# Kernel optimization log

Hardware: AMD Instinct MI355X
Metric: run time of the kernel (lower is better)

## Reference

```python
import jax, jax.numpy as jnp
import numpy as np

N_HEAD, N_MIX, D_MODEL, D_K, D_V = 8, 2, 512, 64, 64
BN_EPS = 1e-5


def avg_pool_3x3_s2(x):
    # AvgPool2d(kernel=3, stride=2, pad=1, count_include_pad=False) on NCHW
    win = (1, 1, 3, 3)
    stride = (1, 1, 2, 2)
    pad = [(0, 0), (0, 0), (1, 1), (1, 1)]
    s = jax.lax.reduce_window(x, 0.0, jax.lax.add, win, stride, pad)
    ones = jnp.ones((1, 1, x.shape[2], x.shape[3]), x.dtype)
    cnt = jax.lax.reduce_window(ones, 0.0, jax.lax.add, win, stride, pad)
    return s / cnt


def conv1x1(x, w, b=None):
    # w: [out_c, in_c]; x: [B, in_c, H, W]
    y = jnp.einsum('oc,bchw->bohw', w, x)
    if b is not None:
        y = y + b[None, :, None, None]
    return y


def setup_inputs() -> dict:
    key = jax.random.key(0)
    ks = jax.random.split(key, 8)
    B, H, W = 2, 56, 56
    std_kq = np.sqrt(2.0 / (D_MODEL + D_K)).astype(np.float32)
    std_v = np.sqrt(2.0 / (D_MODEL + D_V)).astype(np.float32)
    std_mix = np.power(N_MIX, -0.5).astype(np.float32)
    return {
        'x': jax.random.normal(ks[0], (B, D_MODEL, H, W), jnp.float32),
        'w_qs': jax.random.normal(ks[1], (N_HEAD * D_K, D_MODEL), jnp.float32) * std_kq,
        'b_qs': jnp.zeros((N_HEAD * D_K,), jnp.float32),
        'w_vs': jax.random.normal(ks[2], (N_HEAD * D_V, D_MODEL), jnp.float32) * std_v,
        'b_vs': jnp.zeros((N_HEAD * D_V,), jnp.float32),
        'mix_w': jax.random.uniform(ks[3], (N_MIX, D_K), jnp.float32, -std_mix, std_mix),
        'w_out': jax.random.normal(ks[4], (D_MODEL, N_HEAD * D_V), jnp.float32) * 0.02,
        'bn_gamma': jnp.ones((D_MODEL,), jnp.float32),
        'bn_beta': jnp.zeros((D_MODEL,), jnp.float32),
    }


def reference(x, w_qs, b_qs, w_vs, b_vs, mix_w, w_out, bn_gamma, bn_beta):
    B, C, H, W = x.shape
    N = H * W
    m = N_MIX
    d = D_K // m  # per-mixture dim
    temperature = D_K ** 0.5

    px = avg_pool_3x3_s2(x)  # [B, C, H/2, W/2]
    N2 = px.shape[2] * px.shape[3]

    # conv_ks aliases conv_qs in the original (shared weights)
    qt = conv1x1(x, w_qs, b_qs).reshape(B * N_HEAD, D_K, N)
    kt = conv1x1(px, w_qs, b_qs).reshape(B * N_HEAD, D_K, N2)
    vt = conv1x1(px, w_vs, b_vs).reshape(B * N_HEAD, D_V, N2)

    # mixture weights pi: softmax over mixtures of weight @ mean_q
    bar_qt = qt.mean(axis=2)  # [B', D_K]
    pi = jax.nn.softmax(jnp.einsum('md,bd->bm', mix_w, bar_qt), axis=1)  # [B', m]

    q = qt.reshape(B * N_HEAD * m, d, N).transpose(0, 2, 1)  # [B'm, N, d]
    k2 = kt.reshape(B * N_HEAD * m, d, N2)  # [B'm, d, N2]

    attn = jnp.einsum('bnd,bdk->bnk', q, k2) / temperature  # [B'm, N, N2]
    attn = jax.nn.softmax(attn, axis=2)
    # dropout is identity in eval mode
    attn = (attn * pi.reshape(-1, 1, 1)).reshape(B * N_HEAD, m, N, N2).sum(1)

    out = jnp.einsum('bnk,bvk->bnv', attn, vt)  # [B', N, D_V]
    out = out.transpose(0, 2, 1).reshape(B, N_HEAD * D_V, H, W)
    out = conv1x1(out, w_out)  # no bias
    # BatchNorm2d in eval mode: running_mean=0, running_var=1
    inv = 1.0 / jnp.sqrt(jnp.float32(1.0 + BN_EPS))
    out = out * inv * bn_gamma[None, :, None, None] + bn_beta[None, :, None, None]
    return out + x
```

## Files before the change

kernel.cpp:

```cpp
#include <hip/hip_runtime.h>
#include <math.h>

typedef unsigned short u16;
typedef short bf16x8 __attribute__((ext_vector_type(8)));
typedef short bf16x4 __attribute__((ext_vector_type(4)));
typedef float f32x4 __attribute__((ext_vector_type(4)));

#define MFMA(a, b, c) __builtin_amdgcn_mfma_f32_16x16x32_bf16(a, b, c, 0, 0, 0)

#define SCALE_K 0.18033688011112043f

__device__ __forceinline__ float bf2f(u16 v) {
    union { float f; unsigned u; } x;
    x.u = ((unsigned)v) << 16;
    return x.f;
}
__device__ __forceinline__ u16 f2bf(float f) {
    union { float f; unsigned u; } x;
    x.f = f;
    unsigned r = x.u + 0x7FFF + ((x.u >> 16) & 1);
    return (u16)(r >> 16);
}
__device__ __forceinline__ bf16x4 pk4(float a, float b, float c, float d) {
    union { unsigned u[2]; bf16x4 v; } x;
    asm("v_cvt_pk_bf16_f32 %0, %1, %2" : "=v"(x.u[0]) : "v"(a), "v"(b));
    asm("v_cvt_pk_bf16_f32 %0, %1, %2" : "=v"(x.u[1]) : "v"(c), "v"(d));
    return x.v;
}

__global__ __launch_bounds__(256) void cvt_kernel(const float* __restrict__ s0,
                                                  const float* __restrict__ s1,
                                                  const float* __restrict__ s2,
                                                  u16* __restrict__ d0, u16* __restrict__ d1,
                                                  u16* __restrict__ d2) {
    int i = blockIdx.x * 256 + threadIdx.x;
    const float* s = (blockIdx.y == 0) ? s0 : ((blockIdx.y == 1) ? s1 : s2);
    u16* d = (blockIdx.y == 0) ? d0 : ((blockIdx.y == 1) ? d1 : d2);
    d[i] = f2bf(s[i]);
}

__global__ __launch_bounds__(256) void transpose_kernel(const float* __restrict__ x,
                                                        u16* __restrict__ xT) {
    __shared__ u16 tile[64][65];
    int b = blockIdx.z;
    int n0 = blockIdx.x * 64, c0 = blockIdx.y * 64;
    int j = threadIdx.x & 63, q = threadIdx.x >> 6;
    const float* xb = x + b * 512 * 3136;
#pragma unroll
    for (int it = 0; it < 16; ++it) {
        int r = q * 16 + it;
        tile[r][j] = f2bf(xb[(c0 + r) * 3136 + n0 + j]);
    }
    __syncthreads();
    u16* xTb = xT + b * 3136 * 512;
#pragma unroll
    for (int it = 0; it < 16; ++it) {
        int r = q * 16 + it;
        xTb[(n0 + r) * 512 + c0 + j] = tile[j][r];
    }
}

__global__ __launch_bounds__(256) void pool_kernel(const u16* __restrict__ xT,
                                                   u16* __restrict__ pxT) {
    int n2 = blockIdx.x;
    int b = blockIdx.y;
    int t = threadIdx.x;
    int i = n2 / 28, jj = n2 % 28;
    float s0 = 0.f, s1 = 0.f;
    int cnt = 0;
    const u16* xb = xT + b * 3136 * 512;
#pragma unroll
    for (int dr = 0; dr < 3; dr++) {
        int r = 2 * i - 1 + dr;
        if (r < 0 || r >= 56) continue;
#pragma unroll
        for (int dc = 0; dc < 3; dc++) {
            int cc = 2 * jj - 1 + dc;
            if (cc < 0 || cc >= 56) continue;
            const u16* row = xb + (r * 56 + cc) * 512;
            s0 += bf2f(row[t]);
            s1 += bf2f(row[t + 256]);
            cnt++;
        }
    }
    float invc = 1.0f / (float)cnt;
    u16* op = pxT + (b * 784 + n2) * 512;
    op[t] = f2bf(s0 * invc);
    op[t + 256] = f2bf(s1 * invc);
}

__device__ __forceinline__ void gemm_core(const u16* __restrict__ A, int lda, int M,
                                          const u16* __restrict__ BT, int ldb, int Ncol,
                                          int K, int row0, int col0, f32x4 acc[4][4]) {
    int lane = threadIdx.x & 63;
    int lr = lane & 15, lg = lane >> 4;
    int ar[4], bc[4];
#pragma unroll
    for (int i = 0; i < 4; i++) {
        int r = row0 + i * 16 + lr;
        ar[i] = (r < M) ? r : (M - 1);
    }
#pragma unroll
    for (int j = 0; j < 4; j++) {
        int cj = col0 + j * 16 + lr;
        bc[j] = (cj < Ncol) ? cj : (Ncol - 1);
    }
    for (int k = 0; k < K; k += 32) {
        int ko = k + lg * 8;
        bf16x8 af[4], bfr[4];
#pragma unroll
        for (int i = 0; i < 4; i++) af[i] = *(const bf16x8*)(A + ar[i] * lda + ko);
#pragma unroll
        for (int j = 0; j < 4; j++) bfr[j] = *(const bf16x8*)(BT + bc[j] * ldb + ko);
#pragma unroll
        for (int i = 0; i < 4; i++)
#pragma unroll
            for (int j = 0; j < 4; j++) acc[i][j] = MFMA(af[i], bfr[j], acc[i][j]);
    }
}

__global__ __launch_bounds__(256) void gemm_qk(const u16* __restrict__ xT,
                                               const u16* __restrict__ W,
                                               const float* __restrict__ bias,
                                               u16* __restrict__ out, int M, int Npad,
                                               float oscale) {
    int b = blockIdx.z;
    int w = threadIdx.x >> 6;
    int row0 = blockIdx.y * 128 + (w >> 1) * 64;
    int col0 = blockIdx.x * 128 + (w & 1) * 64;
    f32x4 acc[4][4];
#pragma unroll
    for (int i = 0; i < 4; i++)
#pragma unroll
        for (int j = 0; j < 4; j++) acc[i][j] = (f32x4){0.f, 0.f, 0.f, 0.f};
    gemm_core(xT + b * M * 512, 512, M, W, 512, 512, 512, row0, col0, acc);
    int lane = threadIdx.x & 63;
    int lr = lane & 15, lg = lane >> 4;
#pragma unroll
    for (int j = 0; j < 4; j++) {
        int oc = col0 + j * 16 + lr;
        float bs = bias[oc];
        int bh = b * 8 + (oc >> 6), dk = oc & 63;
        u16* op = out + (bh * Npad) * 64 + dk;
#pragma unroll
        for (int i = 0; i < 4; i++) {
#pragma unroll
            for (int r = 0; r < 4; r++) {
                int n = row0 + i * 16 + lg * 4 + r;
                if (n < M) op[n * 64] = f2bf((acc[i][j][r] + bs) * oscale);
                else if (n < Npad) op[n * 64] = 0;
            }
        }
    }
}

__global__ __launch_bounds__(256) void gemm_v(const u16* __restrict__ W,
                                              const u16* __restrict__ pxT,
                                              const float* __restrict__ bias,
                                              u16* __restrict__ vt) {
    int b = blockIdx.z;
    int w = threadIdx.x >> 6;
    int row0 = blockIdx.y * 128 + (w >> 1) * 64;
    int col0 = blockIdx.x * 128 + (w & 1) * 64;
    f32x4 acc[4][4];
#pragma unroll
    for (int i = 0; i < 4; i++)
#pragma unroll
        for (int j = 0; j < 4; j++) acc[i][j] = (f32x4){0.f, 0.f, 0.f, 0.f};
    gemm_core(W, 512, 512, pxT + b * 784 * 512, 512, 784, 512, row0, col0, acc);
    int lane = threadIdx.x & 63;
    int lr = lane & 15, lg = lane >> 4;
#pragma unroll
    for (int i = 0; i < 4; i++) {
#pragma unroll
        for (int r = 0; r < 4; r++) {
            int oc = row0 + i * 16 + lg * 4 + r;
            float bs = bias[oc];
            u16* vp = vt + ((b * 8 + (oc >> 6)) * 64 + (oc & 63)) * 800;
#pragma unroll
            for (int j = 0; j < 4; j++) {
                int n2 = col0 + j * 16 + lr;
                if (n2 < 784) vp[n2] = f2bf(acc[i][j][r] + bs);
                else if (n2 < 800) vp[n2] = 0;
            }
        }
    }
}

__global__ __launch_bounds__(256) void pi_stage1(const u16* __restrict__ qt,
                                                 float* __restrict__ part) {
    __shared__ float red[4][64];
    int chunk = blockIdx.x, bh = blockIdx.y;
    int t = threadIdx.x, dk = t & 63, seg = t >> 6;
    const u16* q = qt + (bh * 3136 + chunk * 112) * 64 + dk;
    float s = 0.f;
    for (int n = seg; n < 112; n += 4) s += bf2f(q[n * 64]);
    red[seg][dk] = s;
    __syncthreads();
    if (t < 64) part[(bh * 28 + chunk) * 64 + t] =
        red[0][t] + red[1][t] + red[2][t] + red[3][t];
}

__global__ __launch_bounds__(64) void pi_stage2(const float* __restrict__ part,
                                                const float* __restrict__ mix_w,
                                                float* __restrict__ pi) {
    int bh = blockIdx.x, lane = threadIdx.x;
    float bar = 0.f;
#pragma unroll
    for (int c = 0; c < 28; c++) bar += part[(bh * 28 + c) * 64 + lane];
    bar *= (1.0f / 3136.0f);
    float l0 = mix_w[lane] * bar;
    float l1 = mix_w[64 + lane] * bar;
#pragma unroll
    for (int d = 1; d < 64; d <<= 1) {
        l0 += __shfl_xor(l0, d);
        l1 += __shfl_xor(l1, d);
    }
    if (lane == 0) {
        float mx = fmaxf(l0, l1);
        float e0 = __expf(l0 - mx), e1 = __expf(l1 - mx);
        float inv = 1.0f / (e0 + e1);
        pi[bh * 2 + 0] = e0 * inv;
        pi[bh * 2 + 1] = e1 * inv;
    }
}

__global__ __launch_bounds__(256) void attn_kernel(const u16* __restrict__ qt,
                                                   const u16* __restrict__ kt,
                                                   const u16* __restrict__ vt,
                                                   const float* __restrict__ pi,
                                                   u16* __restrict__ ao) {
    __shared__ float ldsO[8][16][65];
    __shared__ float ldsL[8][16];
    int w = threadIdx.x >> 6, lane = threadIdx.x & 63;
    int lr = lane & 15, lg = lane >> 4;
    int bh = blockIdx.x & 15;
    int qti = blockIdx.x >> 4;
    int qbase = qti * 16;
    const u16* qp = qt + (bh * 3136 + qbase) * 64;
    const u16* kbase = kt + bh * 800 * 64 + lr * 64 + lg * 8;
    const u16* vbase = vt + bh * 64 * 800 + lr * 800 + lg * 4;

    bf16x8 qf0 = *(const bf16x8*)(qp + lr * 64 + lg * 8);
    bf16x8 qf1 = *(const bf16x8*)(qp + lr * 64 + 32 + lg * 8);

    const f32x4 z4 = {0.f, 0.f, 0.f, 0.f};
    f32x4 O00 = z4, O01 = z4, O02 = z4, O03 = z4;
    f32x4 O10 = z4, O11 = z4, O12 = z4, O13 = z4;
    float ls0 = 0.f, ls1 = 0.f;

    int start = (w == 0) ? 0 : 1 + 6 * w;
    int end = start + ((w == 0) ? 7 : 6);
    for (int c = start; c < end; ++c) {
        int base = c * 32;
        bool tail = (c == 24);
        bf16x8 k00 = *(const bf16x8*)(kbase + base * 64);
        bf16x8 k01 = *(const bf16x8*)(kbase + (base + 16) * 64);
        bf16x8 k10 = *(const bf16x8*)(kbase + base * 64 + 32);
        bf16x8 k11 = *(const bf16x8*)(kbase + (base + 16) * 64 + 32);
        bf16x4 va0 = *(const bf16x4*)(vbase + base);
        bf16x4 va1 = *(const bf16x4*)(vbase + base + 16 * 800);
        bf16x4 va2 = *(const bf16x4*)(vbase + base + 32 * 800);
        bf16x4 va3 = *(const bf16x4*)(vbase + base + 48 * 800);
        bf16x4 vb0 = *(const bf16x4*)(vbase + base + 16);
        bf16x4 vb1 = *(const bf16x4*)(vbase + base + 16 + 16 * 800);
        bf16x4 vb2 = *(const bf16x4*)(vbase + base + 16 + 32 * 800);
        bf16x4 vb3 = *(const bf16x4*)(vbase + base + 16 + 48 * 800);
        union { bf16x4 h[2]; bf16x8 w8; } vv0, vv1, vv2, vv3, pa;
        vv0.h[0] = va0; vv0.h[1] = vb0;
        vv1.h[0] = va1; vv1.h[1] = vb1;
        vv2.h[0] = va2; vv2.h[1] = vb2;
        vv3.h[0] = va3; vv3.h[1] = vb3;
        f32x4 s0 = MFMA(k00, qf0, z4);
        f32x4 s1 = MFMA(k01, qf0, z4);
        float p0 = __builtin_amdgcn_exp2f(s0[0]);
        float p1 = __builtin_amdgcn_exp2f(s0[1]);
        float p2 = __builtin_amdgcn_exp2f(s0[2]);
        float p3 = __builtin_amdgcn_exp2f(s0[3]);
        float p4 = __builtin_amdgcn_exp2f(s1[0]);
        float p5 = __builtin_amdgcn_exp2f(s1[1]);
        float p6 = __builtin_amdgcn_exp2f(s1[2]);
        float p7 = __builtin_amdgcn_exp2f(s1[3]);
        if (tail) { p4 = 0.f; p5 = 0.f; p6 = 0.f; p7 = 0.f; }
        ls0 += ((p0 + p1) + (p2 + p3)) + ((p4 + p5) + (p6 + p7));
        pa.h[0] = pk4(p0, p1, p2, p3);
        pa.h[1] = pk4(p4, p5, p6, p7);
        O00 = MFMA(pa.w8, vv0.w8, O00);
        O01 = MFMA(pa.w8, vv1.w8, O01);
        O02 = MFMA(pa.w8, vv2.w8, O02);
        O03 = MFMA(pa.w8, vv3.w8, O03);
        s0 = MFMA(k10, qf1, z4);
        s1 = MFMA(k11, qf1, z4);
        p0 = __builtin_amdgcn_exp2f(s0[0]);
        p1 = __builtin_amdgcn_exp2f(s0[1]);
        p2 = __builtin_amdgcn_exp2f(s0[2]);
        p3 = __builtin_amdgcn_exp2f(s0[3]);
        p4 = __builtin_amdgcn_exp2f(s1[0]);
        p5 = __builtin_amdgcn_exp2f(s1[1]);
        p6 = __builtin_amdgcn_exp2f(s1[2]);
        p7 = __builtin_amdgcn_exp2f(s1[3]);
        if (tail) { p4 = 0.f; p5 = 0.f; p6 = 0.f; p7 = 0.f; }
        ls1 += ((p0 + p1) + (p2 + p3)) + ((p4 + p5) + (p6 + p7));
        pa.h[0] = pk4(p0, p1, p2, p3);
        pa.h[1] = pk4(p4, p5, p6, p7);
        O10 = MFMA(pa.w8, vv0.w8, O10);
        O11 = MFMA(pa.w8, vv1.w8, O11);
        O12 = MFMA(pa.w8, vv2.w8, O12);
        O13 = MFMA(pa.w8, vv3.w8, O13);
    }

    ls0 += __shfl_xor(ls0, 16);
    ls0 += __shfl_xor(ls0, 32);
    ls1 += __shfl_xor(ls1, 16);
    ls1 += __shfl_xor(ls1, 32);
    if (lane < 16) {
        ldsL[w * 2 + 0][lr] = ls0;
        ldsL[w * 2 + 1][lr] = ls1;
    }
#define PUTO(T, OA, OB)                              \
    {                                                \
        _Pragma("unroll") for (int r = 0; r < 4; r++) { \
            ldsO[w * 2 + 0][lg * 4 + r][(T)*16 + lr] = OA[r]; \
            ldsO[w * 2 + 1][lg * 4 + r][(T)*16 + lr] = OB[r]; \
        }                                            \
    }
    PUTO(0, O00, O10)
    PUTO(1, O01, O11)
    PUTO(2, O02, O12)
    PUTO(3, O03, O13)
#undef PUTO
    __syncthreads();

    float pi0 = pi[bh * 2], pi1 = pi[bh * 2 + 1];
    int col = threadIdx.x & 63, rg = threadIdx.x >> 6;
    int b = bh >> 3, h = bh & 7;
    u16* aop = ao + ((b * 3136 + qbase) * 512) + h * 64;
#pragma unroll
    for (int i = 0; i < 4; i++) {
        int q = rg * 4 + i;
        float l0 = ldsL[0][q] + ldsL[2][q] + ldsL[4][q] + ldsL[6][q];
        float l1 = ldsL[1][q] + ldsL[3][q] + ldsL[5][q] + ldsL[7][q];
        float o0 = ldsO[0][q][col] + ldsO[2][q][col] + ldsO[4][q][col] + ldsO[6][q][col];
        float o1 = ldsO[1][q][col] + ldsO[3][q][col] + ldsO[5][q][col] + ldsO[7][q][col];
        aop[q * 512 + col] = f2bf((pi0 / l0) * o0 + (pi1 / l1) * o1);
    }
}

__global__ __launch_bounds__(256) void gemm_out(const u16* __restrict__ W,
                                                const u16* __restrict__ aoT,
                                                const float* __restrict__ gamma,
                                                const float* __restrict__ beta,
                                                const float* __restrict__ xres,
                                                float* __restrict__ out) {
    int b = blockIdx.z;
    int w = threadIdx.x >> 6;
    int row0 = blockIdx.y * 128 + (w >> 1) * 64;
    int col0 = blockIdx.x * 128 + (w & 1) * 64;
    f32x4 acc[4][4];
#pragma unroll
    for (int i = 0; i < 4; i++)
#pragma unroll
        for (int j = 0; j < 4; j++) acc[i][j] = (f32x4){0.f, 0.f, 0.f, 0.f};
    gemm_core(W, 512, 512, aoT + b * 3136 * 512, 512, 3136, 512, row0, col0, acc);
    const float inv = 0.99999500003749969f;
    int lane = threadIdx.x & 63;
    int lr = lane & 15, lg = lane >> 4;
#pragma unroll
    for (int i = 0; i < 4; i++) {
#pragma unroll
        for (int r = 0; r < 4; r++) {
            int oc = row0 + i * 16 + lg * 4 + r;
            float g = gamma[oc] * inv;
            float bt = beta[oc];
            const float* xp = xres + (b * 512 + oc) * 3136;
            float* op = out + (b * 512 + oc) * 3136;
#pragma unroll
            for (int j = 0; j < 4; j++) {
                int n = col0 + j * 16 + lr;
                if (n < 3136) op[n] = acc[i][j][r] * g + bt + xp[n];
            }
        }
    }
}

extern "C" void kernel_launch(void* const* d_in, const int* in_sizes, int n_in,
                              void* d_out, int out_size, void* d_ws, size_t ws_size,
                              hipStream_t stream) {
    const float* x = (const float*)d_in[0];
    const float* w_qs = (const float*)d_in[1];
    const float* b_qs = (const float*)d_in[2];
    const float* w_vs = (const float*)d_in[3];
    const float* b_vs = (const float*)d_in[4];
    const float* mix_w = (const float*)d_in[5];
    const float* w_out = (const float*)d_in[6];
    const float* gamma = (const float*)d_in[7];
    const float* beta = (const float*)d_in[8];
    float* out = (float*)d_out;

    char* ws = (char*)d_ws;
    u16* xT = (u16*)(ws + 0);
    u16* ao = (u16*)(ws + 0);
    u16* pxT = (u16*)(ws + 6422528);
    u16* qt = (u16*)(ws + 8028160);
    u16* kt = (u16*)(ws + 14450688);
    u16* vt = (u16*)(ws + 16089088);
    u16* wq_b = (u16*)(ws + 17727488);
    u16* wv_b = (u16*)(ws + 18251776);
    u16* wo_b = (u16*)(ws + 18776064);
    float* pi = (float*)(ws + 19300352);
    float* part = (float*)(ws + 19300480);

    hipLaunchKernelGGL(cvt_kernel, dim3(1024, 3), dim3(256), 0, stream, w_qs, w_vs, w_out,
                       wq_b, wv_b, wo_b);
    hipLaunchKernelGGL(transpose_kernel, dim3(49, 8, 2), dim3(256), 0, stream, x, xT);
    hipLaunchKernelGGL(pool_kernel, dim3(784, 2), dim3(256), 0, stream, xT, pxT);
    hipLaunchKernelGGL(gemm_qk, dim3(4, 25, 2), dim3(256), 0, stream, xT, wq_b, b_qs, qt,
                       3136, 3136, 1.0f);
    hipLaunchKernelGGL(gemm_qk, dim3(4, 7, 2), dim3(256), 0, stream, pxT, wq_b, b_qs, kt,
                       784, 800, SCALE_K);
    hipLaunchKernelGGL(gemm_v, dim3(7, 4, 2), dim3(256), 0, stream, wv_b, pxT, b_vs, vt);
    hipLaunchKernelGGL(pi_stage1, dim3(28, 16), dim3(256), 0, stream, qt, part);
    hipLaunchKernelGGL(pi_stage2, dim3(16), dim3(64), 0, stream, part, mix_w, pi);
    hipLaunchKernelGGL(attn_kernel, dim3(3136), dim3(256), 0, stream, qt, kt, vt, pi, ao);
    hipLaunchKernelGGL(gemm_out, dim3(25, 4, 2), dim3(256), 0, stream, wo_b, ao, gamma,
                       beta, x, out);
}
```

Before: 229.1 us.

## Shrink GEMM tiles, split attention waves by mixture, vectorize pooling loads

The GEMM kernels move from 128x128 to 64x64 block tiles (32x32 per wave), which fills more workgroups across the CUs and lowers register pressure, at the cost of more redundant global loads. The attention kernel now gives each wave one mixture half of the head dimension and half of the key range, instead of having every wave cover both mixtures over a sixth of the keys. This removes the unrolled dual-mixture code and halves the LDS reduction buffers. The pooling kernel reads and writes two bf16 values per 32-bit access.

```diff
diff --git a/kernel.cpp b/kernel.cpp
--- a/kernel.cpp
+++ b/kernel.cpp
@@ -2,6 +2,7 @@
 #include <math.h>
 
 typedef unsigned short u16;
+typedef unsigned int u32;
 typedef short bf16x8 __attribute__((ext_vector_type(8)));
 typedef short bf16x4 __attribute__((ext_vector_type(4)));
 typedef float f32x4 __attribute__((ext_vector_type(4)));
@@ -11,18 +12,18 @@
 #define SCALE_K 0.18033688011112043f
 
 __device__ __forceinline__ float bf2f(u16 v) {
-    union { float f; unsigned u; } x;
-    x.u = ((unsigned)v) << 16;
+    union { float f; u32 u; } x;
+    x.u = ((u32)v) << 16;
     return x.f;
 }
 __device__ __forceinline__ u16 f2bf(float f) {
-    union { float f; unsigned u; } x;
+    union { float f; u32 u; } x;
     x.f = f;
-    unsigned r = x.u + 0x7FFF + ((x.u >> 16) & 1);
+    u32 r = x.u + 0x7FFF + ((x.u >> 16) & 1);
     return (u16)(r >> 16);
 }
 __device__ __forceinline__ bf16x4 pk4(float a, float b, float c, float d) {
-    union { unsigned u[2]; bf16x4 v; } x;
+    union { u32 u[2]; bf16x4 v; } x;
     asm("v_cvt_pk_bf16_f32 %0, %1, %2" : "=v"(x.u[0]) : "v"(a), "v"(b));
     asm("v_cvt_pk_bf16_f32 %0, %1, %2" : "=v"(x.u[1]) : "v"(c), "v"(d));
     return x.v;
@@ -77,45 +78,44 @@
         for (int dc = 0; dc < 3; dc++) {
             int cc = 2 * jj - 1 + dc;
             if (cc < 0 || cc >= 56) continue;
-            const u16* row = xb + (r * 56 + cc) * 512;
-            s0 += bf2f(row[t]);
-            s1 += bf2f(row[t + 256]);
+            u32 pr = *(const u32*)(xb + (r * 56 + cc) * 512 + 2 * t);
+            s0 += bf2f((u16)pr);
+            s1 += bf2f((u16)(pr >> 16));
             cnt++;
         }
     }
     float invc = 1.0f / (float)cnt;
-    u16* op = pxT + (b * 784 + n2) * 512;
-    op[t] = f2bf(s0 * invc);
-    op[t + 256] = f2bf(s1 * invc);
-}
-
-__device__ __forceinline__ void gemm_core(const u16* __restrict__ A, int lda, int M,
-                                          const u16* __restrict__ BT, int ldb, int Ncol,
-                                          int K, int row0, int col0, f32x4 acc[4][4]) {
+    u32 o = (u32)f2bf(s0 * invc) | ((u32)f2bf(s1 * invc) << 16);
+    *(u32*)(pxT + (b * 784 + n2) * 512 + 2 * t) = o;
+}
+
+__device__ __forceinline__ void gemm_core32(const u16* __restrict__ A, int lda, int M,
+                                            const u16* __restrict__ BT, int ldb, int Ncol,
+                                            int K, int row0, int col0, f32x4 acc[2][2]) {
     int lane = threadIdx.x & 63;
     int lr = lane & 15, lg = lane >> 4;
-    int ar[4], bc[4];
-#pragma unroll
-    for (int i = 0; i < 4; i++) {
+    int ar[2], bc[2];
+#pragma unroll
+    for (int i = 0; i < 2; i++) {
         int r = row0 + i * 16 + lr;
         ar[i] = (r < M) ? r : (M - 1);
     }
 #pragma unroll
-    for (int j = 0; j < 4; j++) {
+    for (int j = 0; j < 2; j++) {
         int cj = col0 + j * 16 + lr;
         bc[j] = (cj < Ncol) ? cj : (Ncol - 1);
     }
+#pragma unroll 2
     for (int k = 0; k < K; k += 32) {
         int ko = k + lg * 8;
-        bf16x8 af[4], bfr[4];
-#pragma unroll
-        for (int i = 0; i < 4; i++) af[i] = *(const bf16x8*)(A + ar[i] * lda + ko);
-#pragma unroll
-        for (int j = 0; j < 4; j++) bfr[j] = *(const bf16x8*)(BT + bc[j] * ldb + ko);
-#pragma unroll
-        for (int i = 0; i < 4; i++)
-#pragma unroll
-            for (int j = 0; j < 4; j++) acc[i][j] = MFMA(af[i], bfr[j], acc[i][j]);
+        bf16x8 a0 = *(const bf16x8*)(A + ar[0] * lda + ko);
+        bf16x8 a1 = *(const bf16x8*)(A + ar[1] * lda + ko);
+        bf16x8 b0 = *(const bf16x8*)(BT + bc[0] * ldb + ko);
+        bf16x8 b1 = *(const bf16x8*)(BT + bc[1] * ldb + ko);
+        acc[0][0] = MFMA(a0, b0, acc[0][0]);
+        acc[0][1] = MFMA(a0, b1, acc[0][1]);
+        acc[1][0] = MFMA(a1, b0, acc[1][0]);
+        acc[1][1] = MFMA(a1, b1, acc[1][1]);
     }
 }
 
@@ -126,24 +126,24 @@
                                                float oscale) {
     int b = blockIdx.z;
     int w = threadIdx.x >> 6;
-    int row0 = blockIdx.y * 128 + (w >> 1) * 64;
-    int col0 = blockIdx.x * 128 + (w & 1) * 64;
-    f32x4 acc[4][4];
-#pragma unroll
-    for (int i = 0; i < 4; i++)
-#pragma unroll
-        for (int j = 0; j < 4; j++) acc[i][j] = (f32x4){0.f, 0.f, 0.f, 0.f};
-    gemm_core(xT + b * M * 512, 512, M, W, 512, 512, 512, row0, col0, acc);
+    int row0 = blockIdx.y * 64 + (w >> 1) * 32;
+    int col0 = blockIdx.x * 64 + (w & 1) * 32;
+    f32x4 acc[2][2];
+#pragma unroll
+    for (int i = 0; i < 2; i++)
+#pragma unroll
+        for (int j = 0; j < 2; j++) acc[i][j] = (f32x4){0.f, 0.f, 0.f, 0.f};
+    gemm_core32(xT + b * M * 512, 512, M, W, 512, 512, 512, row0, col0, acc);
     int lane = threadIdx.x & 63;
     int lr = lane & 15, lg = lane >> 4;
 #pragma unroll
-    for (int j = 0; j < 4; j++) {
+    for (int j = 0; j < 2; j++) {
         int oc = col0 + j * 16 + lr;
         float bs = bias[oc];
         int bh = b * 8 + (oc >> 6), dk = oc & 63;
         u16* op = out + (bh * Npad) * 64 + dk;
 #pragma unroll
-        for (int i = 0; i < 4; i++) {
+        for (int i = 0; i < 2; i++) {
 #pragma unroll
             for (int r = 0; r < 4; r++) {
                 int n = row0 + i * 16 + lg * 4 + r;
@@ -160,25 +160,25 @@
                                               u16* __restrict__ vt) {
     int b = blockIdx.z;
     int w = threadIdx.x >> 6;
-    int row0 = blockIdx.y * 128 + (w >> 1) * 64;
-    int col0 = blockIdx.x * 128 + (w & 1) * 64;
-    f32x4 acc[4][4];
-#pragma unroll
-    for (int i = 0; i < 4; i++)
-#pragma unroll
-        for (int j = 0; j < 4; j++) acc[i][j] = (f32x4){0.f, 0.f, 0.f, 0.f};
-    gemm_core(W, 512, 512, pxT + b * 784 * 512, 512, 784, 512, row0, col0, acc);
+    int row0 = blockIdx.y * 64 + (w >> 1) * 32;
+    int col0 = blockIdx.x * 64 + (w & 1) * 32;
+    f32x4 acc[2][2];
+#pragma unroll
+    for (int i = 0; i < 2; i++)
+#pragma unroll
+        for (int j = 0; j < 2; j++) acc[i][j] = (f32x4){0.f, 0.f, 0.f, 0.f};
+    gemm_core32(W, 512, 512, pxT + b * 784 * 512, 512, 784, 512, row0, col0, acc);
     int lane = threadIdx.x & 63;
     int lr = lane & 15, lg = lane >> 4;
 #pragma unroll
-    for (int i = 0; i < 4; i++) {
+    for (int i = 0; i < 2; i++) {
 #pragma unroll
         for (int r = 0; r < 4; r++) {
             int oc = row0 + i * 16 + lg * 4 + r;
             float bs = bias[oc];
             u16* vp = vt + ((b * 8 + (oc >> 6)) * 64 + (oc & 63)) * 800;
 #pragma unroll
-            for (int j = 0; j < 4; j++) {
+            for (int j = 0; j < 2; j++) {
                 int n2 = col0 + j * 16 + lr;
                 if (n2 < 784) vp[n2] = f2bf(acc[i][j][r] + bs);
                 else if (n2 < 800) vp[n2] = 0;
@@ -230,34 +230,30 @@
                                                    const u16* __restrict__ vt,
                                                    const float* __restrict__ pi,
                                                    u16* __restrict__ ao) {
-    __shared__ float ldsO[8][16][65];
-    __shared__ float ldsL[8][16];
+    __shared__ float ldsO[4][16][66];
+    __shared__ float ldsL[4][16];
     int w = threadIdx.x >> 6, lane = threadIdx.x & 63;
     int lr = lane & 15, lg = lane >> 4;
     int bh = blockIdx.x & 15;
     int qti = blockIdx.x >> 4;
     int qbase = qti * 16;
+    int m = w >> 1, half = w & 1;
     const u16* qp = qt + (bh * 3136 + qbase) * 64;
-    const u16* kbase = kt + bh * 800 * 64 + lr * 64 + lg * 8;
+    const u16* kbase = kt + bh * 800 * 64 + lr * 64 + m * 32 + lg * 8;
     const u16* vbase = vt + bh * 64 * 800 + lr * 800 + lg * 4;
 
-    bf16x8 qf0 = *(const bf16x8*)(qp + lr * 64 + lg * 8);
-    bf16x8 qf1 = *(const bf16x8*)(qp + lr * 64 + 32 + lg * 8);
+    bf16x8 qf = *(const bf16x8*)(qp + lr * 64 + m * 32 + lg * 8);
 
     const f32x4 z4 = {0.f, 0.f, 0.f, 0.f};
-    f32x4 O00 = z4, O01 = z4, O02 = z4, O03 = z4;
-    f32x4 O10 = z4, O11 = z4, O12 = z4, O13 = z4;
-    float ls0 = 0.f, ls1 = 0.f;
-
-    int start = (w == 0) ? 0 : 1 + 6 * w;
-    int end = start + ((w == 0) ? 7 : 6);
-    for (int c = start; c < end; ++c) {
+    f32x4 O0 = z4, O1 = z4, O2 = z4, O3 = z4;
+    float ls = 0.f;
+
+    int cs = half ? 13 : 0, ce = half ? 25 : 13;
+    for (int c = cs; c < ce; ++c) {
         int base = c * 32;
         bool tail = (c == 24);
-        bf16x8 k00 = *(const bf16x8*)(kbase + base * 64);
-        bf16x8 k01 = *(const bf16x8*)(kbase + (base + 16) * 64);
-        bf16x8 k10 = *(const bf16x8*)(kbase + base * 64 + 32);
-        bf16x8 k11 = *(const bf16x8*)(kbase + (base + 16) * 64 + 32);
+        bf16x8 k0 = *(const bf16x8*)(kbase + base * 64);
+        bf16x8 k1 = *(const bf16x8*)(kbase + (base + 16) * 64);
         bf16x4 va0 = *(const bf16x4*)(vbase + base);
         bf16x4 va1 = *(const bf16x4*)(vbase + base + 16 * 800);
         bf16x4 va2 = *(const bf16x4*)(vbase + base + 32 * 800);
@@ -271,8 +267,8 @@
         vv1.h[0] = va1; vv1.h[1] = vb1;
         vv2.h[0] = va2; vv2.h[1] = vb2;
         vv3.h[0] = va3; vv3.h[1] = vb3;
-        f32x4 s0 = MFMA(k00, qf0, z4);
-        f32x4 s1 = MFMA(k01, qf0, z4);
+        f32x4 s0 = MFMA(k0, qf, z4);
+        f32x4 s1 = MFMA(k1, qf, z4);
         float p0 = __builtin_amdgcn_exp2f(s0[0]);
         float p1 = __builtin_amdgcn_exp2f(s0[1]);
         float p2 = __builtin_amdgcn_exp2f(s0[2]);
@@ -282,53 +278,25 @@
         float p6 = __builtin_amdgcn_exp2f(s1[2]);
         float p7 = __builtin_amdgcn_exp2f(s1[3]);
         if (tail) { p4 = 0.f; p5 = 0.f; p6 = 0.f; p7 = 0.f; }
-        ls0 += ((p0 + p1) + (p2 + p3)) + ((p4 + p5) + (p6 + p7));
+        ls += ((p0 + p1) + (p2 + p3)) + ((p4 + p5) + (p6 + p7));
         pa.h[0] = pk4(p0, p1, p2, p3);
         pa.h[1] = pk4(p4, p5, p6, p7);
-        O00 = MFMA(pa.w8, vv0.w8, O00);
-        O01 = MFMA(pa.w8, vv1.w8, O01);
-        O02 = MFMA(pa.w8, vv2.w8, O02);
-        O03 = MFMA(pa.w8, vv3.w8, O03);
-        s0 = MFMA(k10, qf1, z4);
-        s1 = MFMA(k11, qf1, z4);
-        p0 = __builtin_amdgcn_exp2f(s0[0]);
-        p1 = __builtin_amdgcn_exp2f(s0[1]);
-        p2 = __builtin_amdgcn_exp2f(s0[2]);
-        p3 = __builtin_amdgcn_exp2f(s0[3]);
-        p4 = __builtin_amdgcn_exp2f(s1[0]);
-        p5 = __builtin_amdgcn_exp2f(s1[1]);
-        p6 = __builtin_amdgcn_exp2f(s1[2]);
-        p7 = __builtin_amdgcn_exp2f(s1[3]);
-        if (tail) { p4 = 0.f; p5 = 0.f; p6 = 0.f; p7 = 0.f; }
-        ls1 += ((p0 + p1) + (p2 + p3)) + ((p4 + p5) + (p6 + p7));
-        pa.h[0] = pk4(p0, p1, p2, p3);
-        pa.h[1] = pk4(p4, p5, p6, p7);
-        O10 = MFMA(pa.w8, vv0.w8, O10);
-        O11 = MFMA(pa.w8, vv1.w8, O11);
-        O12 = MFMA(pa.w8, vv2.w8, O12);
-        O13 = MFMA(pa.w8, vv3.w8, O13);
-    }
-
-    ls0 += __shfl_xor(ls0, 16);
-    ls0 += __shfl_xor(ls0, 32);
-    ls1 += __shfl_xor(ls1, 16);
-    ls1 += __shfl_xor(ls1, 32);
-    if (lane < 16) {
-        ldsL[w * 2 + 0][lr] = ls0;
-        ldsL[w * 2 + 1][lr] = ls1;
-    }
-#define PUTO(T, OA, OB)                              \
-    {                                                \
-        _Pragma("unroll") for (int r = 0; r < 4; r++) { \
-            ldsO[w * 2 + 0][lg * 4 + r][(T)*16 + lr] = OA[r]; \
-            ldsO[w * 2 + 1][lg * 4 + r][(T)*16 + lr] = OB[r]; \
-        }                                            \
-    }
-    PUTO(0, O00, O10)
-    PUTO(1, O01, O11)
-    PUTO(2, O02, O12)
-    PUTO(3, O03, O13)
-#undef PUTO
+        O0 = MFMA(pa.w8, vv0.w8, O0);
+        O1 = MFMA(pa.w8, vv1.w8, O1);
+        O2 = MFMA(pa.w8, vv2.w8, O2);
+        O3 = MFMA(pa.w8, vv3.w8, O3);
+    }
+
+    ls += __shfl_xor(ls, 16);
+    ls += __shfl_xor(ls, 32);
+    if (lane < 16) ldsL[w][lr] = ls;
+#pragma unroll
+    for (int r = 0; r < 4; r++) {
+        ldsO[w][lg * 4 + r][0 * 16 + lr] = O0[r];
+        ldsO[w][lg * 4 + r][1 * 16 + lr] = O1[r];
+        ldsO[w][lg * 4 + r][2 * 16 + lr] = O2[r];
+        ldsO[w][lg * 4 + r][3 * 16 + lr] = O3[r];
+    }
     __syncthreads();
 
     float pi0 = pi[bh * 2], pi1 = pi[bh * 2 + 1];
@@ -338,10 +306,10 @@
 #pragma unroll
     for (int i = 0; i < 4; i++) {
         int q = rg * 4 + i;
-        float l0 = ldsL[0][q] + ldsL[2][q] + ldsL[4][q] + ldsL[6][q];
-        float l1 = ldsL[1][q] + ldsL[3][q] + ldsL[5][q] + ldsL[7][q];
-        float o0 = ldsO[0][q][col] + ldsO[2][q][col] + ldsO[4][q][col] + ldsO[6][q][col];
-        float o1 = ldsO[1][q][col] + ldsO[3][q][col] + ldsO[5][q][col] + ldsO[7][q][col];
+        float l0 = ldsL[0][q] + ldsL[1][q];
+        float l1 = ldsL[2][q] + ldsL[3][q];
+        float o0 = ldsO[0][q][col] + ldsO[1][q][col];
+        float o1 = ldsO[2][q][col] + ldsO[3][q][col];
         aop[q * 512 + col] = f2bf((pi0 / l0) * o0 + (pi1 / l1) * o1);
     }
 }
@@ -354,19 +322,19 @@
                                                 float* __restrict__ out) {
     int b = blockIdx.z;
     int w = threadIdx.x >> 6;
-    int row0 = blockIdx.y * 128 + (w >> 1) * 64;
-    int col0 = blockIdx.x * 128 + (w & 1) * 64;
-    f32x4 acc[4][4];
-#pragma unroll
-    for (int i = 0; i < 4; i++)
-#pragma unroll
-        for (int j = 0; j < 4; j++) acc[i][j] = (f32x4){0.f, 0.f, 0.f, 0.f};
-    gemm_core(W, 512, 512, aoT + b * 3136 * 512, 512, 3136, 512, row0, col0, acc);
+    int row0 = blockIdx.y * 64 + (w >> 1) * 32;
+    int col0 = blockIdx.x * 64 + (w & 1) * 32;
+    f32x4 acc[2][2];
+#pragma unroll
+    for (int i = 0; i < 2; i++)
+#pragma unroll
+        for (int j = 0; j < 2; j++) acc[i][j] = (f32x4){0.f, 0.f, 0.f, 0.f};
+    gemm_core32(W, 512, 512, aoT + b * 3136 * 512, 512, 3136, 512, row0, col0, acc);
     const float inv = 0.99999500003749969f;
     int lane = threadIdx.x & 63;
     int lr = lane & 15, lg = lane >> 4;
 #pragma unroll
-    for (int i = 0; i < 4; i++) {
+    for (int i = 0; i < 2; i++) {
 #pragma unroll
         for (int r = 0; r < 4; r++) {
             int oc = row0 + i * 16 + lg * 4 + r;
@@ -375,7 +343,7 @@
             const float* xp = xres + (b * 512 + oc) * 3136;
             float* op = out + (b * 512 + oc) * 3136;
 #pragma unroll
-            for (int j = 0; j < 4; j++) {
+            for (int j = 0; j < 2; j++) {
                 int n = col0 + j * 16 + lr;
                 if (n < 3136) op[n] = acc[i][j][r] * g + bt + xp[n];
             }
@@ -414,14 +382,14 @@
                        wq_b, wv_b, wo_b);
     hipLaunchKernelGGL(transpose_kernel, dim3(49, 8, 2), dim3(256), 0, stream, x, xT);
     hipLaunchKernelGGL(pool_kernel, dim3(784, 2), dim3(256), 0, stream, xT, pxT);
-    hipLaunchKernelGGL(gemm_qk, dim3(4, 25, 2), dim3(256), 0, stream, xT, wq_b, b_qs, qt,
+    hipLaunchKernelGGL(gemm_qk, dim3(8, 49, 2), dim3(256), 0, stream, xT, wq_b, b_qs, qt,
                        3136, 3136, 1.0f);
-    hipLaunchKernelGGL(gemm_qk, dim3(4, 7, 2), dim3(256), 0, stream, pxT, wq_b, b_qs, kt,
+    hipLaunchKernelGGL(gemm_qk, dim3(8, 13, 2), dim3(256), 0, stream, pxT, wq_b, b_qs, kt,
                        784, 800, SCALE_K);
-    hipLaunchKernelGGL(gemm_v, dim3(7, 4, 2), dim3(256), 0, stream, wv_b, pxT, b_vs, vt);
+    hipLaunchKernelGGL(gemm_v, dim3(13, 8, 2), dim3(256), 0, stream, wv_b, pxT, b_vs, vt);
     hipLaunchKernelGGL(pi_stage1, dim3(28, 16), dim3(256), 0, stream, qt, part);
     hipLaunchKernelGGL(pi_stage2, dim3(16), dim3(64), 0, stream, part, mix_w, pi);
     hipLaunchKernelGGL(attn_kernel, dim3(3136), dim3(256), 0, stream, qt, kt, vt, pi, ao);
-    hipLaunchKernelGGL(gemm_out, dim3(25, 4, 2), dim3(256), 0, stream, wo_b, ao, gamma,
+    hipLaunchKernelGGL(gemm_out, dim3(49, 8, 2), dim3(256), 0, stream, wo_b, ao, gamma,
                        beta, x, out);
 }
```

Result: slower. 237.4 us (+3.6%).
